# Optimization experiments

Hardware: AMD Instinct MI355X
Metric: run time of the kernel (lower is better)

## Reference

```python
import jax, jax.numpy as jnp
import numpy as np

TEMPERATURE = 1.0
CHUNK = 128  # node-block size for the curvature pass


def setup_inputs() -> dict:
    key = jax.random.key(0)
    k1, k2 = jax.random.split(key)
    N, D = 4096, 64
    x = jax.random.normal(k1, (N, D), dtype=jnp.float32)
    # sparse binary adjacency (avg degree ~16) + ring so min degree >= 2
    A = (jax.random.uniform(k2, (N, N)) < 0.004).astype(jnp.float32)
    i = jnp.arange(N)
    A = A.at[i, i].set(0.0)
    A = A.at[i, (i + 1) % N].set(1.0)
    A = A.at[(i + 1) % N, i].set(1.0)
    return {"node_embeddings": x, "adj_matrix": A}


def _physics_components(x, A):
    N, d = x.shape
    mask = A > 0
    deg = jnp.sum(A, axis=-1)                      # [N]

    # ---- total energy ----
    kinetic = jnp.sum(x * x, axis=-1)
    nb = A @ x                                     # neighbor aggregate [N,d]
    potential = -jnp.sum(x * nb, axis=-1)
    total_energy = kinetic + potential / (deg + 1e-8)

    # ---- local entropy over neighbor similarities ----
    xn = x / jnp.maximum(jnp.linalg.norm(x, axis=-1, keepdims=True), 1e-12)
    S = xn @ xn.T                                  # cosine sims [N,N]
    logits = jnp.where(mask, S / TEMPERATURE, -1e30)
    P = jax.nn.softmax(logits, axis=-1)            # masked softmax per row
    local_entropy = -jnp.sum(jnp.where(mask, P * jnp.log(P + 1e-8), 0.0), axis=-1)

    # ---- equilibrium deviation (5-NN local mean in embedding space) ----
    sq = jnp.sum(x * x, axis=-1)
    D2 = jnp.maximum(sq[:, None] + sq[None, :] - 2.0 * (x @ x.T), 1e-12)
    dist = jnp.sqrt(D2)                            # [N,N]
    _, idx = jax.lax.top_k(-dist, 6)               # smallest 6 (self first)
    local_means = jnp.mean(x[idx[:, 1:]], axis=1)  # [N,d]
    gdev = jnp.linalg.norm(x - jnp.mean(x, axis=0, keepdims=True), axis=-1)
    ldev = jnp.linalg.norm(x - local_means, axis=-1)
    equilibrium_deviation = 0.6 * gdev + 0.4 * ldev

    # ---- structural centrality ----
    en = jnp.linalg.norm(x, axis=-1)
    structural_centrality = 0.5 * deg / (N - 1) + 0.5 * en / jnp.max(en)

    # ---- information flow: unbiased var of neighbor sims ----
    ms = jnp.sum(jnp.where(mask, S, 0.0), axis=-1) / deg
    information_flow = jnp.sum(jnp.where(mask, (S - ms[:, None]) ** 2, 0.0), axis=-1) / (deg - 1.0)

    # ---- stability: 1/(1 + mean unbiased var of neighbor embeddings) ----
    m1 = nb / deg[:, None]
    ex2 = A @ (x * x)
    var_dim = (ex2 - deg[:, None] * m1 * m1) / (deg - 1.0)[:, None]
    stability = 1.0 / (1.0 + jnp.mean(var_dim, axis=-1))

    # ---- discrete curvature: 1 - mean pairwise cos angle of centered neighbors ----
    # mean_{j<k} u_j.u_k = (||sum u||^2 - sum ||u||^2) / (deg*(deg-1))
    def body(_, ids):
        xb = x[ids]                                 # [B,d]
        mb = mask[ids]                              # [B,N]
        c = x[None, :, :] - xb[:, None, :]          # [B,N,d]
        nrm = jnp.sqrt(jnp.maximum(jnp.sum(c * c, -1), 1e-12))
        u = jnp.where(mb[..., None], c / jnp.maximum(nrm, 1e-8)[..., None], 0.0)
        s = jnp.sum(u, axis=1)                      # [B,d]
        ssq = jnp.sum(u * u, axis=(1, 2))           # [B]
        db = jnp.sum(mb.astype(x.dtype), axis=-1)
        mean_cos = (jnp.sum(s * s, -1) - ssq) / (db * (db - 1.0))
        return None, 1.0 - mean_cos

    _, curv = jax.lax.scan(body, None, jnp.arange(N).reshape(-1, CHUNK))
    graph_curvature = curv.reshape(N)

    return (total_energy, local_entropy, equilibrium_deviation,
            structural_centrality, information_flow, stability, graph_curvature)


def reference(node_embeddings, adj_matrix):
    return _physics_components(node_embeddings, adj_matrix)
```

## Files before the change

kernel.cpp:

```cpp
#include <hip/hip_runtime.h>
#include <math.h>

#define NN 4096
#define DD 64
#define NSPLIT 16
#define JW 256

typedef _Float16 half8 __attribute__((ext_vector_type(8)));
typedef float f32x4 __attribute__((ext_vector_type(4)));

__device__ __forceinline__ unsigned sxu(unsigned v, int o){
  return (unsigned)__shfl_xor((int)v, o, 64);
}
__device__ __forceinline__ unsigned umn(unsigned a, unsigned b){ return a<b?a:b; }
__device__ __forceinline__ unsigned umx(unsigned a, unsigned b){ return a<b?b:a; }
__device__ __forceinline__ unsigned med3u(unsigned a, unsigned b, unsigned c){
  unsigned r; asm("v_med3_u32 %0, %1, %2, %3" : "=v"(r) : "v"(a), "v"(b), "v"(c)); return r;
}
__device__ __forceinline__ unsigned min3u(unsigned a, unsigned b, unsigned c){
  unsigned r; asm("v_min3_u32 %0, %1, %2, %3" : "=v"(r) : "v"(a), "v"(b), "v"(c)); return r;
}

__device__ __forceinline__ unsigned packkey32(float m, int j){
  float q = fmaf(m, 2048.f, 524288.f);
  q = fminf(fmaxf(q, 0.f), 1048575.f);
  return (((unsigned)q) << 12) | (unsigned)j;
}

__device__ __forceinline__ void ins5u(unsigned k, unsigned b[5]){
  unsigned nb0 = umn(k, b[0]);
  b[4] = med3u(k, b[3], b[4]);
  b[3] = med3u(k, b[2], b[3]);
  b[2] = med3u(k, b[1], b[2]);
  b[1] = med3u(k, b[0], b[1]);
  b[0] = nb0;
}

__device__ __forceinline__ void mergeStage32(unsigned b[5], int st){
  unsigned p0=sxu(b[0],st),p1=sxu(b[1],st),p2=sxu(b[2],st),p3=sxu(b[3],st),p4=sxu(b[4],st);
  unsigned o0=umn(b[0],p0);
  unsigned o1=min3u(b[1],p1, umx(b[0],p0));
  unsigned o2=min3u(b[2],p2, umn(umx(b[0],p1),umx(b[1],p0)));
  unsigned o3=min3u(b[3],p3, min3u(umx(b[0],p2), umx(b[1],p1), umx(b[2],p0)));
  unsigned o4=min3u(b[4],p4, umn(umn(umx(b[0],p3),umx(b[1],p2)),
                                 umn(umx(b[2],p1),umx(b[3],p0))));
  b[0]=o0;b[1]=o1;b[2]=o2;b[3]=o3;b[4]=o4;
}

__device__ __forceinline__ void mergeLocal32(const unsigned a[5], const unsigned c[5], unsigned b[5]){
  b[0]=umn(a[0],c[0]);
  b[1]=min3u(a[1],c[1], umx(a[0],c[0]));
  b[2]=min3u(a[2],c[2], umn(umx(a[0],c[1]),umx(a[1],c[0])));
  b[3]=min3u(a[3],c[3], min3u(umx(a[0],c[2]), umx(a[1],c[1]), umx(a[2],c[0])));
  b[4]=min3u(a[4],c[4], umn(umn(umx(a[0],c[3]),umx(a[1],c[2])),
                            umn(umx(a[2],c[1]),umx(a[3],c[0]))));
}

__global__ __launch_bounds__(256) void k_prec(const float* __restrict__ x,
                      float* __restrict__ sq,
                      _Float16* __restrict__ xh, _Float16* __restrict__ xl,
                      float* __restrict__ msum_part, float* __restrict__ maxsq_part){
  __shared__ float part[4][64];
  __shared__ float mxp[4];
  const int w = threadIdx.x>>6, lane = threadIdx.x&63;
  const int n0 = blockIdx.x*16 + w*4;
  float v0 = x[(size_t)(n0+0)*DD + lane];
  float v1 = x[(size_t)(n0+1)*DD + lane];
  float v2 = x[(size_t)(n0+2)*DD + lane];
  float v3 = x[(size_t)(n0+3)*DD + lane];
  float s0=v0*v0, s1=v1*v1, s2=v2*v2, s3=v3*v3;
#pragma unroll
  for(int o=1;o<64;o<<=1){
    s0 += __shfl_xor(s0,o,64); s1 += __shfl_xor(s1,o,64);
    s2 += __shfl_xor(s2,o,64); s3 += __shfl_xor(s3,o,64);
  }
  float vv[4] = {v0,v1,v2,v3};
  float ss[4] = {s0,s1,s2,s3};
#pragma unroll
  for(int q=0;q<4;q++){
    float v = vv[q];
    _Float16 h = (_Float16)v;
    _Float16 l = (_Float16)(v - (float)h);
    xh[(size_t)(n0+q)*DD+lane] = h;
    xl[(size_t)(n0+q)*DD+lane] = l;
    if(lane==0) sq[n0+q]=ss[q];
  }
  if(lane==0) mxp[w] = fmaxf(fmaxf(s0,s1), fmaxf(s2,s3));
  part[w][lane] = v0+v1+v2+v3; __syncthreads();
  if(w==0){
    msum_part[blockIdx.x*64 + lane] = part[0][lane]+part[1][lane]+part[2][lane]+part[3][lane];
    if(lane==0) maxsq_part[blockIdx.x] = fmaxf(fmaxf(mxp[0],mxp[1]), fmaxf(mxp[2],mxp[3]));
  }
}

__device__ __forceinline__ f32x4 gram6(const half8 J[4],
    half8 Ih0, half8 Ih1, half8 Il0, half8 Il1){
  const f32x4 z = {0.f,0.f,0.f,0.f};
  f32x4 a1 = __builtin_amdgcn_mfma_f32_16x16x32_f16(J[0], Ih0, z, 0,0,0);
  f32x4 a2 = __builtin_amdgcn_mfma_f32_16x16x32_f16(J[2], Ih0, z, 0,0,0);
  a1 = __builtin_amdgcn_mfma_f32_16x16x32_f16(J[1], Ih1, a1, 0,0,0);
  a2 = __builtin_amdgcn_mfma_f32_16x16x32_f16(J[3], Ih1, a2, 0,0,0);
  a1 = __builtin_amdgcn_mfma_f32_16x16x32_f16(J[0], Il0, a1, 0,0,0);
  a1 = __builtin_amdgcn_mfma_f32_16x16x32_f16(J[1], Il1, a1, 0,0,0);
  return a1 + a2;
}

__global__ __launch_bounds__(256, 4) void k_mega(
    const float* __restrict__ x, const float* __restrict__ A,
    const float* __restrict__ sq,
    const _Float16* __restrict__ xh, const _Float16* __restrict__ xl,
    unsigned* __restrict__ cand,
    const float* __restrict__ msum_part, const float* __restrict__ maxsq_part,
    float* __restrict__ msum, float* __restrict__ max_sq, float* __restrict__ deg_out,
    float* __restrict__ o_te, float* __restrict__ o_ent,
    float* __restrict__ o_if, float* __restrict__ o_st, float* __restrict__ o_cv)
{
  __shared__ __align__(16) char smem[16384];
  const int bid = blockIdx.x;
  const int tid = threadIdx.x;
  const int w = tid>>6, lane = tid&63;

  if(bid == 0){
    float* rr = (float*)smem;
    float* rm = (float*)(smem + 1024);
    float s = 0.f;
    for(int p=w; p<256; p+=4) s += msum_part[p*64 + lane];
    rr[w*64 + lane] = s;
    float m = maxsq_part[w*64 + lane];
#pragma unroll
    for(int o=1;o<64;o<<=1) m = fmaxf(m, __shfl_xor(m,o,64));
    if(lane==0) rm[w] = m;
    __syncthreads();
    if(w==0){
      msum[lane] = rr[0*64+lane]+rr[1*64+lane]+rr[2*64+lane]+rr[3*64+lane];
      if(lane==0) max_sq[0] = fmaxf(fmaxf(rm[0],rm[1]), fmaxf(rm[2],rm[3]));
    }
    return;
  }

  const int t = bid - 1;
  if((t & 1) == 0){
    int*   nbrw  = (int*)smem + w*128;
    float* Svalw = (float*)(smem + 2048) + w*128;
    const int i = (t>>1)*4 + w;
    const float xid = x[(size_t)i*DD + lane];
    const float sqi = sq[i];
    const float eni = sqrtf(sqi);
    const float4* A4 = (const float4*)(A + (size_t)i*NN);
    const unsigned long long below = (1ull << lane) - 1ull;

    int base = 0;
#define COMPACT(VAL, JJ) { \
    bool p_ = (VAL) > 0.f; \
    unsigned long long m_ = __ballot(p_); \
    int ofs_ = base + (int)__popcll(m_ & below); \
    if(p_ && ofs_ < 128) nbrw[ofs_] = (JJ); \
    base += (int)__popcll(m_); \
  }
    for(int ch=0; ch<4; ++ch){
      float4 av[4];
#pragma unroll
      for(int qq=0; qq<4; ++qq) av[qq] = A4[lane + 64*(ch*4+qq)];
#pragma unroll
      for(int qq=0; qq<4; ++qq){
        int jb = 4*(lane + 64*(ch*4+qq));
        COMPACT(av[qq].x, jb+0);
        COMPACT(av[qq].y, jb+1);
        COMPACT(av[qq].z, jb+2);
        COMPACT(av[qq].w, jb+3);
      }
    }
#undef COMPACT
    const int deg = base;

    const float degf = (float)deg;
    const int dmax = min(deg, 128);
    float nb_d=0.f, ex2_d=0.f, s_d=0.f, ssq=0.f;

    for(int c0=0; c0<dmax; c0+=8){
      int jq[8]; float aq[8], qq[8];
#pragma unroll
      for(int q=0;q<8;q++) jq[q] = nbrw[min(c0+q, dmax-1)];
#pragma unroll
      for(int q=0;q<8;q++) aq[q] = x[(size_t)jq[q]*DD + lane];
#pragma unroll
      for(int q=0;q<8;q++) qq[q] = sq[jq[q]];
      asm volatile("" :: "v"(aq[0]), "v"(aq[1]), "v"(aq[2]), "v"(aq[3]),
                         "v"(aq[4]), "v"(aq[5]), "v"(aq[6]), "v"(aq[7]));
      float p[8];
#pragma unroll
      for(int q=0;q<8;q++) p[q] = xid*aq[q];
#pragma unroll
      for(int o=1;o<64;o<<=1){
#pragma unroll
        for(int q=0;q<8;q++) p[q] += __shfl_xor(p[q],o,64);
      }
#pragma unroll
      for(int q=0;q<8;q++){
        const bool valid = (c0+q) < deg;
        float c2 = fmaxf(sqi + qq[q] - 2.0f*p[q], 1e-12f);
        float inv = 1.0f/fmaxf(sqrtf(c2), 1e-8f);
        nb_d  += valid ? aq[q] : 0.f;
        ex2_d += valid ? aq[q]*aq[q] : 0.f;
        s_d   += valid ? (aq[q]-xid)*inv : 0.f;
        ssq   += valid ? c2*inv*inv : 0.f;
        if(valid && lane==q) Svalw[c0+q] = p[q]/(eni*sqrtf(qq[q]));
      }
    }

    float t0 = xid*nb_d;
    float m1 = nb_d/degf;
    float t1 = (ex2_d - degf*m1*m1)/(degf-1.0f);
    float t2 = s_d*s_d;
    float t3 = 0.f, t4 = 0.f;
    for(int s=lane; s<dmax; s+=64){ float v=Svalw[s]; t3 += expf(v); t4 += v; }
#pragma unroll
    for(int o=1;o<64;o<<=1){
      t0 += __shfl_xor(t0,o,64); t1 += __shfl_xor(t1,o,64); t2 += __shfl_xor(t2,o,64);
      t3 += __shfl_xor(t3,o,64); t4 += __shfl_xor(t4,o,64);
    }
    const float pot = t0, varm = t1*(1.0f/DD), s2 = t2, se = t3, ms = t4/degf;

    float e0=0.f, e1=0.f;
    const float inv_se = 1.0f/se;
    for(int s=lane; s<dmax; s+=64){
      float v = Svalw[s];
      float pp = expf(v)*inv_se;
      e0 -= pp*logf(pp + 1e-8f);
      float dv = v-ms; e1 += dv*dv;
    }
#pragma unroll
    for(int o=1;o<64;o<<=1){ e0 += __shfl_xor(e0,o,64); e1 += __shfl_xor(e1,o,64); }

    if(lane==0){
      o_te[i]  = sqi - pot/(degf + 1e-8f);
      o_ent[i] = e0;
      o_if[i]  = e1/(degf-1.0f);
      o_st[i]  = 1.0f/(1.0f + varm);
      o_cv[i]  = 1.0f - (s2 - ssq)/(degf*(degf-1.0f));
      deg_out[i] = degf;
    }
  } else {
    _Float16* jHi = (_Float16*)smem;
    _Float16* jLo = (_Float16*)(smem + 8192);
    const int kid = t >> 1;
    const int split = kid & (NSPLIT-1);
    const int strip = (kid >> 4)*4 + w;
    const int ibase = strip*16, j0 = split*JW;
    const int col = lane & 15, kg = lane >> 4;
    const int vo = col*DD + kg*8;
    const int myi = ibase + col;

#define STAGE(CH) { \
    _Pragma("unroll") \
    for(int q_=0;q_<2;q_++){ \
      int g_ = q_*256 + tid; \
      int r_ = g_ >> 3; \
      int c_ = (g_ & 7) ^ (r_ & 7); \
      const _Float16* sH_ = xh + (size_t)(j0 + (CH)*64 + r_)*DD + c_*8; \
      const _Float16* sL_ = xl + (size_t)(j0 + (CH)*64 + r_)*DD + c_*8; \
      __builtin_amdgcn_global_load_lds( \
        (const __attribute__((address_space(1))) unsigned int*)sH_, \
        (__attribute__((address_space(3))) unsigned int*)(jHi + g_*8), 16, 0, 0); \
      __builtin_amdgcn_global_load_lds( \
        (const __attribute__((address_space(1))) unsigned int*)sL_, \
        (__attribute__((address_space(3))) unsigned int*)(jLo + g_*8), 16, 0, 0); \
    } }

    const _Float16* pih = xh + (size_t)ibase*DD + vo;
    const _Float16* pil = xl + (size_t)ibase*DD + vo;
    const half8 Ih0 = *(const half8*)(pih);
    const half8 Ih1 = *(const half8*)(pih+32);
    const half8 Il0 = *(const half8*)(pil);
    const half8 Il1 = *(const half8*)(pil+32);

    unsigned bA[5], bB[5];
#pragma unroll
    for(int k=0;k<5;k++){ bA[k]=0xFFFFFFFFu; bB[k]=0xFFFFFFFFu; }

#pragma unroll
    for(int ch=0; ch<4; ch++){
      STAGE(ch);
      const int jb0 = j0 + ch*64 + kg*4;
      float4 sq0 = *(const float4*)(sq + jb0);
      float4 sq1 = *(const float4*)(sq + jb0 + 16);
      float4 sq2 = *(const float4*)(sq + jb0 + 32);
      float4 sq3 = *(const float4*)(sq + jb0 + 48);
      __syncthreads();

      half8 JT[4];
#define TILE(TT, SQV, LIST) { \
      const int rl_ = (TT)*16 + col; \
      const int sw_ = rl_ & 7; \
      JT[0] = *(const half8*)(jHi + (rl_*8 + ( kg      ^ sw_))*8); \
      JT[1] = *(const half8*)(jHi + (rl_*8 + ((kg + 4) ^ sw_))*8); \
      JT[2] = *(const half8*)(jLo + (rl_*8 + ( kg      ^ sw_))*8); \
      JT[3] = *(const half8*)(jLo + (rl_*8 + ((kg + 4) ^ sw_))*8); \
      f32x4 d_ = gram6(JT, Ih0, Ih1, Il0, Il1); \
      float sv_[4] = {SQV.x, SQV.y, SQV.z, SQV.w}; \
      const int jt0_ = jb0 + (TT)*16; \
      _Pragma("unroll") \
      for(int r_=0;r_<4;r_++){ \
        unsigned kk_ = packkey32(fmaf(-2.0f, d_[r_], sv_[r_]), jt0_+r_); \
        kk_ = (jt0_+r_==myi) ? 0xFFFFFFFFu : kk_; \
        ins5u(kk_, LIST); \
      } }

      TILE(0, sq0, bA);
      TILE(1, sq1, bB);
      TILE(2, sq2, bA);
      TILE(3, sq3, bB);
#undef TILE
      __syncthreads();
    }
#undef STAGE

    unsigned b[5];
    mergeLocal32(bA, bB, b);
    mergeStage32(b, 16);
    mergeStage32(b, 32);

    if(kg==0){
#pragma unroll
      for(int k=0;k<5;k++)
        cand[((size_t)myi*NSPLIT + split)*5 + k] = b[k];
    }
  }
}

__global__ __launch_bounds__(256) void k_nnsel(
    const float* __restrict__ x, const unsigned* __restrict__ cand,
    const float* __restrict__ msum, const float* __restrict__ max_sq,
    const float* __restrict__ deg, const float* __restrict__ sq,
    float* __restrict__ o_eq, float* __restrict__ o_sc)
{
  const int w = threadIdx.x>>6, l = threadIdx.x&63;
  const int i = blockIdx.x*4 + w;
  const unsigned* cr = cand + (size_t)i*(NSPLIT*5);
  unsigned c0 = cr[l];
  unsigned c1 = (l < 16) ? cr[64+l] : 0xFFFFFFFFu;

  int sel[5];
#pragma unroll
  for(int k=0;k<5;k++){
    unsigned d = umn(c0,c1);
#pragma unroll
    for(int o=1;o<64;o<<=1) d = umn(d, sxu(d,o));
    sel[k] = (int)(d & 0xFFFu);
    if(c0==d) c0=0xFFFFFFFFu;
    else if(c1==d) c1=0xFFFFFFFFu;
  }

  float smv=0.f;
#pragma unroll
  for(int k=0;k<5;k++) smv += x[(size_t)sel[k]*DD + l];
  float xiv = x[(size_t)i*DD + l];
  float lv = xiv - smv*0.2f;
  float gv = xiv - msum[l]*(1.0f/NN);
  float pl = lv*lv, pg = gv*gv;
#pragma unroll
  for(int o=1;o<64;o<<=1){ pl += __shfl_xor(pl,o,64); pg += __shfl_xor(pg,o,64); }
  if(l==0){
    o_eq[i] = 0.6f*sqrtf(pg) + 0.4f*sqrtf(pl);
    o_sc[i] = 0.5f*deg[i]/(float)(NN-1) + 0.5f*sqrtf(sq[i])/sqrtf(max_sq[0]);
  }
}

extern "C" void kernel_launch(void* const* d_in, const int* in_sizes, int n_in,
                              void* d_out, int out_size, void* d_ws, size_t ws_size,
                              hipStream_t stream) {
  const float* x = (const float*)d_in[0];
  const float* A = (const float*)d_in[1];
  float* out = (float*)d_out;
  float* ws  = (float*)d_ws;
  float*     sq        = ws;
  float*     msum      = ws + 4096;
  float*     max_sq    = ws + 4160;
  float*     deg       = ws + 4224;
  float*     msum_part = ws + 8320;
  float*     maxsq_part= ws + 24704;
  _Float16*  xh        = (_Float16*)(ws + 24960);
  _Float16*  xl        = (_Float16*)(ws + 156032);
  unsigned*  cand      = (unsigned*)(ws + 287104);

  k_prec<<<NN/16, 256, 0, stream>>>(x, sq, xh, xl, msum_part, maxsq_part);
  k_mega<<<NN/2 + 1, 256, 0, stream>>>(x, A, sq, xh, xl, cand,
                                       msum_part, maxsq_part, msum, max_sq, deg,
                                       out, out+NN, out+4*NN, out+5*NN, out+6*NN);
  k_nnsel<<<NN/4, 256, 0, stream>>>(x, cand, msum, max_sq, deg, sq,
                                    out+2*NN, out+3*NN);
}
```

Measured before the change: 57.45 us.

## Split kNN distance work into 64 column splits with one chunk per block

Raises the kNN column-split count from 16 to 64 so that each kNN block handles a single 64-column chunk. The per-block staging loop and its repeated barriers disappear, and the grid interleaves one node-stats block with four kNN blocks (5*NN/4+1 blocks total). The selection kernel now merges 320 candidates per row instead of 80, and the candidate buffer grows to match. The intent is more parallelism and shorter blocks for better latency hiding. The cost is more launched blocks, repeated I-fragment loads, and larger candidate traffic and merge work.

```diff
diff --git a/kernel.cpp b/kernel.cpp
--- a/kernel.cpp
+++ b/kernel.cpp
@@ -3,8 +3,8 @@
 
 #define NN 4096
 #define DD 64
-#define NSPLIT 16
-#define JW 256
+#define NSPLIT 64
+#define JW 64
 
 typedef _Float16 half8 __attribute__((ext_vector_type(8)));
 typedef float f32x4 __attribute__((ext_vector_type(4)));
@@ -139,10 +139,10 @@
   }
 
   const int t = bid - 1;
-  if((t & 1) == 0){
+  if(t % 5 == 0){
     int*   nbrw  = (int*)smem + w*128;
     float* Svalw = (float*)(smem + 2048) + w*128;
-    const int i = (t>>1)*4 + w;
+    const int i = (t/5)*4 + w;
     const float xid = x[(size_t)i*DD + lane];
     const float sqi = sq[i];
     const float eni = sqrtf(sqi);
@@ -243,29 +243,28 @@
   } else {
     _Float16* jHi = (_Float16*)smem;
     _Float16* jLo = (_Float16*)(smem + 8192);
-    const int kid = t >> 1;
+    const int kid = (t/5)*4 + (t%5) - 1;
     const int split = kid & (NSPLIT-1);
-    const int strip = (kid >> 4)*4 + w;
+    const int strip = (kid >> 6)*4 + w;
     const int ibase = strip*16, j0 = split*JW;
     const int col = lane & 15, kg = lane >> 4;
     const int vo = col*DD + kg*8;
     const int myi = ibase + col;
 
-#define STAGE(CH) { \
-    _Pragma("unroll") \
-    for(int q_=0;q_<2;q_++){ \
-      int g_ = q_*256 + tid; \
-      int r_ = g_ >> 3; \
-      int c_ = (g_ & 7) ^ (r_ & 7); \
-      const _Float16* sH_ = xh + (size_t)(j0 + (CH)*64 + r_)*DD + c_*8; \
-      const _Float16* sL_ = xl + (size_t)(j0 + (CH)*64 + r_)*DD + c_*8; \
-      __builtin_amdgcn_global_load_lds( \
-        (const __attribute__((address_space(1))) unsigned int*)sH_, \
-        (__attribute__((address_space(3))) unsigned int*)(jHi + g_*8), 16, 0, 0); \
-      __builtin_amdgcn_global_load_lds( \
-        (const __attribute__((address_space(1))) unsigned int*)sL_, \
-        (__attribute__((address_space(3))) unsigned int*)(jLo + g_*8), 16, 0, 0); \
-    } }
+#pragma unroll
+    for(int q_=0;q_<2;q_++){
+      int g_ = q_*256 + tid;
+      int r_ = g_ >> 3;
+      int c_ = (g_ & 7) ^ (r_ & 7);
+      const _Float16* sH_ = xh + (size_t)(j0 + r_)*DD + c_*8;
+      const _Float16* sL_ = xl + (size_t)(j0 + r_)*DD + c_*8;
+      __builtin_amdgcn_global_load_lds(
+        (const __attribute__((address_space(1))) unsigned int*)sH_,
+        (__attribute__((address_space(3))) unsigned int*)(jHi + g_*8), 16, 0, 0);
+      __builtin_amdgcn_global_load_lds(
+        (const __attribute__((address_space(1))) unsigned int*)sL_,
+        (__attribute__((address_space(3))) unsigned int*)(jLo + g_*8), 16, 0, 0);
+    }
 
     const _Float16* pih = xh + (size_t)ibase*DD + vo;
     const _Float16* pil = xl + (size_t)ibase*DD + vo;
@@ -274,46 +273,41 @@
     const half8 Il0 = *(const half8*)(pil);
     const half8 Il1 = *(const half8*)(pil+32);
 
+    const int jb0 = j0 + kg*4;
+    float4 sq0 = *(const float4*)(sq + jb0);
+    float4 sq1 = *(const float4*)(sq + jb0 + 16);
+    float4 sq2 = *(const float4*)(sq + jb0 + 32);
+    float4 sq3 = *(const float4*)(sq + jb0 + 48);
+
     unsigned bA[5], bB[5];
 #pragma unroll
     for(int k=0;k<5;k++){ bA[k]=0xFFFFFFFFu; bB[k]=0xFFFFFFFFu; }
 
-#pragma unroll
-    for(int ch=0; ch<4; ch++){
-      STAGE(ch);
-      const int jb0 = j0 + ch*64 + kg*4;
-      float4 sq0 = *(const float4*)(sq + jb0);
-      float4 sq1 = *(const float4*)(sq + jb0 + 16);
-      float4 sq2 = *(const float4*)(sq + jb0 + 32);
-      float4 sq3 = *(const float4*)(sq + jb0 + 48);
-      __syncthreads();
-
-      half8 JT[4];
+    __syncthreads();
+
+    half8 JT[4];
 #define TILE(TT, SQV, LIST) { \
-      const int rl_ = (TT)*16 + col; \
-      const int sw_ = rl_ & 7; \
-      JT[0] = *(const half8*)(jHi + (rl_*8 + ( kg      ^ sw_))*8); \
-      JT[1] = *(const half8*)(jHi + (rl_*8 + ((kg + 4) ^ sw_))*8); \
-      JT[2] = *(const half8*)(jLo + (rl_*8 + ( kg      ^ sw_))*8); \
-      JT[3] = *(const half8*)(jLo + (rl_*8 + ((kg + 4) ^ sw_))*8); \
-      f32x4 d_ = gram6(JT, Ih0, Ih1, Il0, Il1); \
-      float sv_[4] = {SQV.x, SQV.y, SQV.z, SQV.w}; \
-      const int jt0_ = jb0 + (TT)*16; \
-      _Pragma("unroll") \
-      for(int r_=0;r_<4;r_++){ \
-        unsigned kk_ = packkey32(fmaf(-2.0f, d_[r_], sv_[r_]), jt0_+r_); \
-        kk_ = (jt0_+r_==myi) ? 0xFFFFFFFFu : kk_; \
-        ins5u(kk_, LIST); \
-      } }
-
-      TILE(0, sq0, bA);
-      TILE(1, sq1, bB);
-      TILE(2, sq2, bA);
-      TILE(3, sq3, bB);
+    const int rl_ = (TT)*16 + col; \
+    const int sw_ = rl_ & 7; \
+    JT[0] = *(const half8*)(jHi + (rl_*8 + ( kg      ^ sw_))*8); \
+    JT[1] = *(const half8*)(jHi + (rl_*8 + ((kg + 4) ^ sw_))*8); \
+    JT[2] = *(const half8*)(jLo + (rl_*8 + ( kg      ^ sw_))*8); \
+    JT[3] = *(const half8*)(jLo + (rl_*8 + ((kg + 4) ^ sw_))*8); \
+    f32x4 d_ = gram6(JT, Ih0, Ih1, Il0, Il1); \
+    float sv_[4] = {SQV.x, SQV.y, SQV.z, SQV.w}; \
+    const int jt0_ = jb0 + (TT)*16; \
+    _Pragma("unroll") \
+    for(int r_=0;r_<4;r_++){ \
+      unsigned kk_ = packkey32(fmaf(-2.0f, d_[r_], sv_[r_]), jt0_+r_); \
+      kk_ = (jt0_+r_==myi) ? 0xFFFFFFFFu : kk_; \
+      ins5u(kk_, LIST); \
+    } }
+
+    TILE(0, sq0, bA);
+    TILE(1, sq1, bB);
+    TILE(2, sq2, bA);
+    TILE(3, sq3, bB);
 #undef TILE
-      __syncthreads();
-    }
-#undef STAGE
 
     unsigned b[5];
     mergeLocal32(bA, bB, b);
@@ -337,18 +331,20 @@
   const int w = threadIdx.x>>6, l = threadIdx.x&63;
   const int i = blockIdx.x*4 + w;
   const unsigned* cr = cand + (size_t)i*(NSPLIT*5);
-  unsigned c0 = cr[l];
-  unsigned c1 = (l < 16) ? cr[64+l] : 0xFFFFFFFFu;
+  unsigned c0 = cr[l], c1 = cr[64+l], c2 = cr[128+l], c3 = cr[192+l], c4 = cr[256+l];
 
   int sel[5];
 #pragma unroll
   for(int k=0;k<5;k++){
-    unsigned d = umn(c0,c1);
+    unsigned d = umn(min3u(c0,c1,c2), umn(c3,c4));
 #pragma unroll
     for(int o=1;o<64;o<<=1) d = umn(d, sxu(d,o));
     sel[k] = (int)(d & 0xFFFu);
     if(c0==d) c0=0xFFFFFFFFu;
     else if(c1==d) c1=0xFFFFFFFFu;
+    else if(c2==d) c2=0xFFFFFFFFu;
+    else if(c3==d) c3=0xFFFFFFFFu;
+    else if(c4==d) c4=0xFFFFFFFFu;
   }
 
   float smv=0.f;
@@ -384,9 +380,9 @@
   unsigned*  cand      = (unsigned*)(ws + 287104);
 
   k_prec<<<NN/16, 256, 0, stream>>>(x, sq, xh, xl, msum_part, maxsq_part);
-  k_mega<<<NN/2 + 1, 256, 0, stream>>>(x, A, sq, xh, xl, cand,
-                                       msum_part, maxsq_part, msum, max_sq, deg,
-                                       out, out+NN, out+4*NN, out+5*NN, out+6*NN);
+  k_mega<<<5*NN/4 + 1, 256, 0, stream>>>(x, A, sq, xh, xl, cand,
+                                         msum_part, maxsq_part, msum, max_sq, deg,
+                                         out, out+NN, out+4*NN, out+5*NN, out+6*NN);
   k_nnsel<<<NN/4, 256, 0, stream>>>(x, cand, msum, max_sq, deg, sq,
                                     out+2*NN, out+3*NN);
 }
```

Result: no change. 56.80 us (-1.1%).
